# Kernel optimization log

Measured on AMD Instinct MI355X. Metric: run time of the kernel, lower is better.

## Reference

```python
import jax, jax.numpy as jnp
import numpy as np
from jax import lax

B, S, MEL, DM, DI, N, K, R, H, V = 2, 2048, 80, 512, 1024, 16, 4, 32, 8, 10000


def setup_inputs() -> dict:
    ks = iter(jax.random.split(jax.random.key(0), 48))
    r = lambda sh, s=0.02: jax.random.normal(next(ks), sh, jnp.float32) * s
    inp = {"mel": jax.random.normal(next(ks), (B, S, MEL), jnp.float32)}
    inp["mel_w"] = r((DM, MEL)); inp["mel_b"] = r((DM,))
    inp["attn_in_w"] = r((3 * DM, DM)); inp["attn_in_b"] = r((3 * DM,))
    inp["attn_out_w"] = r((DM, DM)); inp["attn_out_b"] = r((DM,))
    inp["ln1_g"] = jnp.ones((DM,)); inp["ln1_b"] = jnp.zeros((DM,))
    inp["ln2_g"] = jnp.ones((DM,)); inp["ln2_b"] = jnp.zeros((DM,))
    for p in ("fm", "bm"):
        inp[p + "_in_w"] = r((2 * DI, DM))
        inp[p + "_conv_w"] = r((DI, K), 0.2)
        inp[p + "_conv_b"] = r((DI,), 0.1)
        inp[p + "_x_w"] = r((R + 2 * N, DI))
        inp[p + "_dt_w"] = r((DI, R), 0.1)
        inp[p + "_dt_b"] = r((DI,), 0.1)
        inp[p + "_A_log"] = jnp.log(jnp.tile(jnp.arange(1, N + 1, dtype=jnp.float32), (DI, 1)))
        inp[p + "_D"] = jnp.ones((DI,))
        inp[p + "_out_w"] = r((DM, DI))
    inp["bim_w"] = r((DM, 2 * DM)); inp["bim_b"] = r((DM,))
    inp["out_w"] = r((V, DM)); inp["out_b"] = r((V,))
    return inp


def _ln(x, g, b):
    mu = x.mean(-1, keepdims=True)
    var = ((x - mu) ** 2).mean(-1, keepdims=True)
    return (x - mu) * lax.rsqrt(var + 1e-5) * g + b


def _mha(x, in_w, in_b, out_w, out_b):
    # torch nn.MultiheadAttention default batch_first=False:
    # axis0 = sequence (here the batch dim B), axis1 = batch (here S). Faithful to source.
    L, Nb, E = x.shape
    hd = E // H
    qkv = x @ in_w.T + in_b
    q, k, v = jnp.split(qkv, 3, axis=-1)
    q = q.reshape(L, Nb, H, hd)
    k = k.reshape(L, Nb, H, hd)
    v = v.reshape(L, Nb, H, hd)
    sc = jnp.einsum('lnhd,mnhd->nhlm', q, k) / np.float32(np.sqrt(hd))
    a = jax.nn.softmax(sc, axis=-1)
    o = jnp.einsum('nhlm,mnhd->lnhd', a, v).reshape(L, Nb, E)
    return o @ out_w.T + out_b


def _mamba(x, in_w, conv_w, conv_b, x_w, dt_w, dt_b, A_log, Dp, out_w):
    # mamba_ssm Mamba block: in_proj -> causal depthwise conv + silu -> x_proj ->
    # softplus(dt_proj) -> selective scan -> gate by silu(z) -> out_proj
    Bb, L, _ = x.shape
    xa, z = jnp.split(x @ in_w.T, 2, axis=-1)  # [B,L,DI] each
    xc = lax.conv_general_dilated(xa.transpose(0, 2, 1), conv_w[:, None, :], (1,), [(K - 1, 0)],
                                  dimension_numbers=('NCH', 'OIH', 'NCH'), feature_group_count=DI)
    xc = jax.nn.silu(xc + conv_b[None, :, None]).transpose(0, 2, 1)  # [B,L,DI]
    dbl = xc @ x_w.T  # [B,L,R+2N]
    dt, Bm, Cm = dbl[..., :R], dbl[..., R:R + N], dbl[..., R + N:]
    dt = jax.nn.softplus(dt @ dt_w.T + dt_b)  # [B,L,DI]
    A = -jnp.exp(A_log)  # [DI,N]

    def step(h, ins):
        dt_t, B_t, C_t, x_t = ins  # [B,DI],[B,N],[B,N],[B,DI]
        h = jnp.exp(dt_t[..., None] * A) * h + (dt_t * x_t)[..., None] * B_t[:, None, :]
        return h, jnp.einsum('bdn,bn->bd', h, C_t)

    h0 = jnp.zeros((Bb, DI, N), x.dtype)
    _, ys = lax.scan(step, h0, (dt.transpose(1, 0, 2), Bm.transpose(1, 0, 2),
                                Cm.transpose(1, 0, 2), xc.transpose(1, 0, 2)))
    y = ys.transpose(1, 0, 2) + xc * Dp
    y = y * jax.nn.silu(z)
    return y @ out_w.T


def reference(mel, mel_w, mel_b, attn_in_w, attn_in_b, attn_out_w, attn_out_b,
              ln1_g, ln1_b, ln2_g, ln2_b,
              fm_in_w, fm_conv_w, fm_conv_b, fm_x_w, fm_dt_w, fm_dt_b, fm_A_log, fm_D, fm_out_w,
              bm_in_w, bm_conv_w, bm_conv_b, bm_x_w, bm_dt_w, bm_dt_b, bm_A_log, bm_D, bm_out_w,
              bim_w, bim_b, out_w, out_b):
    x = mel @ mel_w.T + mel_b  # [B,S,DM]
    x = _ln(x + _mha(x, attn_in_w, attn_in_b, attn_out_w, attn_out_b), ln1_g, ln1_b)
    fwd = _mamba(x, fm_in_w, fm_conv_w, fm_conv_b, fm_x_w, fm_dt_w, fm_dt_b, fm_A_log, fm_D, fm_out_w)
    bwd = jnp.flip(_mamba(jnp.flip(x, 1), bm_in_w, bm_conv_w, bm_conv_b, bm_x_w, bm_dt_w, bm_dt_b, bm_A_log, bm_D, bm_out_w), 1)
    m = jnp.concatenate([fwd, bwd], axis=-1) @ bim_w.T + bim_b
    x = _ln(x + m, ln2_g, ln2_b)
    return x @ out_w.T + out_b  # [B,S,V]
```

## Files before the change

### kernel.cpp

```cpp
#include <hip/hip_runtime.h>
#include <hip/hip_bf16.h>
#include <math.h>

#define SEQ 2048

typedef __attribute__((ext_vector_type(4))) float f32x4;
typedef __attribute__((ext_vector_type(8))) short bf16x8s;
typedef __attribute__((ext_vector_type(8))) unsigned short ushort8;
typedef __attribute__((ext_vector_type(2))) unsigned int uint2v;

__device__ __forceinline__ short f2bf(float f) {
  union { float f; unsigned u; } c; c.f = f;
  unsigned u = c.u;
  u += 0x7fffu + ((u >> 16) & 1u);
  return (short)(u >> 16);
}
__device__ __forceinline__ float bf2f(unsigned short u) {
  union { unsigned u; float f; } c; c.u = ((unsigned)u) << 16; return c.f;
}

__device__ __forceinline__ void lds_load16(const void* g, void* s) {
  __builtin_amdgcn_global_load_lds(
      (const __attribute__((address_space(1))) void*)g,
      (__attribute__((address_space(3))) void*)s, 16, 0, 0);
}

template<int EPI, int OUTBF, int AFLIP1 = 0>
__launch_bounds__(256)
__global__ void gemm_bf16(const unsigned short* A, const unsigned short* B,
                          void* Cv, const float* __restrict__ bias,
                          int M, int N, int K, int lda, int ldb, int ldc, int nbn,
                          const unsigned short* A1, const unsigned short* B1, void* C1) {
  __shared__ char smem[67584];

  if (blockIdx.y) { A = A1; B = B1; Cv = C1; }
  const bool aflip = AFLIP1 && blockIdx.y;

  const int nwg = gridDim.x;
  const int g = blockIdx.x;
  const int q = nwg >> 3, r = nwg & 7;
  const int xcd = g & 7, cidx = g >> 3;
  const int wg = (xcd < r ? xcd * (q + 1) : r * (q + 1) + (xcd - r) * q) + cidx;
  const int sup = nbn << 2;
  const int bmg = wg / sup, rem = wg % sup;
  const int bn = rem >> 2;
  const int bm = (bmg << 2) + (rem & 3);
  const int m0 = bm * 128, n0 = bn * 128;

  const int tid = threadIdx.x, lane = tid & 63, wave = tid >> 6;
  const int wr = (wave >> 1) * 64, wc = (wave & 1) * 64;
  const int fr = lane & 15, fq = lane >> 4;
  const int srow = tid >> 3;
  const int scc  = tid & 7;

  f32x4 acc[4][4] = {};
  const int nkt = K >> 6;

  auto STAGE = [&](int buf, int kt) {
    const int k0 = kt << 6;
    unsigned short* sAb = (unsigned short*)(smem + buf * 32768);
    unsigned short* sBb = (unsigned short*)(smem + buf * 32768 + 16384);
    #pragma unroll
    for (int j = 0; j < 4; j++) {
      int lrow = j * 32 + srow;
      int gcol = (scc ^ (lrow & 7)) * 8;
      int arow = m0 + lrow;
      if (AFLIP1) {
        if (aflip) arow = (arow & ~(SEQ - 1)) | ((SEQ - 1) - (arow & (SEQ - 1)));
      }
      lds_load16(A + (size_t)arow * lda + k0 + gcol, &sAb[(j * 256 + wave * 64) * 8]);
    }
    #pragma unroll
    for (int j = 0; j < 4; j++) {
      int lrow = j * 32 + srow;
      int gcol = (scc ^ (lrow & 7)) * 8;
      int grow = n0 + lrow; if (grow >= N) grow = N - 1;
      lds_load16(B + (size_t)grow * ldb + k0 + gcol, &sBb[(j * 256 + wave * 64) * 8]);
    }
  };

  STAGE(0, 0);

  int cur = 0;
  for (int kt = 0; kt < nkt; kt++) {
    if (kt + 1 < nkt) {
      STAGE(cur ^ 1, kt + 1);
      asm volatile("s_waitcnt vmcnt(8)" ::: "memory");
    } else {
      asm volatile("s_waitcnt vmcnt(0)" ::: "memory");
    }
    __builtin_amdgcn_s_barrier();
    __builtin_amdgcn_sched_barrier(0);
    const unsigned short* As = (const unsigned short*)(smem + cur * 32768);
    const unsigned short* Bs = (const unsigned short*)(smem + cur * 32768 + 16384);
    #pragma unroll
    for (int ks = 0; ks < 2; ks++) {
      bf16x8s af[4], bfv[4];
      #pragma unroll
      for (int i = 0; i < 4; i++) {
        int ra = wr + i * 16 + fr;
        af[i] = *(const bf16x8s*)&As[ra * 64 + (((ks << 2) + fq) ^ (ra & 7)) * 8];
      }
      #pragma unroll
      for (int i = 0; i < 4; i++) {
        int rb = wc + i * 16 + fr;
        bfv[i] = *(const bf16x8s*)&Bs[rb * 64 + (((ks << 2) + fq) ^ (rb & 7)) * 8];
      }
      #pragma unroll
      for (int i = 0; i < 4; i++)
        #pragma unroll
        for (int j = 0; j < 4; j++)
          acc[i][j] = __builtin_amdgcn_mfma_f32_16x16x32_bf16(af[i], bfv[j], acc[i][j], 0, 0, 0);
    }
    __builtin_amdgcn_s_barrier();
    cur ^= 1;
  }

  float* ct = (float*)smem;
  #pragma unroll
  for (int i = 0; i < 4; i++)
    #pragma unroll
    for (int j = 0; j < 4; j++)
      #pragma unroll
      for (int r4 = 0; r4 < 4; r4++)
        ct[(wr + i * 16 + fq * 4 + r4) * 132 + wc + j * 16 + fr] = acc[i][j][r4];
  __syncthreads();
  const int half = lane >> 5;
  const int col4 = (lane & 31) * 4;
  const int cn = n0 + col4;
  #pragma unroll
  for (int it = 0; it < 16; it++) {
    int row = wave * 32 + it * 2 + half;
    f32x4 v = *(const f32x4*)&ct[row * 132 + col4];
    if (cn < N) {
      if (EPI >= 1) {
        f32x4 b4 = *(const f32x4*)&bias[cn];
        #pragma unroll
        for (int j = 0; j < 4; j++) v[j] += b4[j];
      }
      if (OUTBF) {
        unsigned short h0 = (unsigned short)f2bf(v[0]), h1 = (unsigned short)f2bf(v[1]);
        unsigned short h2 = (unsigned short)f2bf(v[2]), h3 = (unsigned short)f2bf(v[3]);
        uint2v o = { (unsigned)h0 | ((unsigned)h1 << 16), (unsigned)h2 | ((unsigned)h3 << 16) };
        *(uint2v*)((unsigned short*)Cv + (size_t)(m0 + row) * ldc + cn) = o;
      } else {
        float* dst = (float*)Cv + (size_t)(m0 + row) * ldc + cn;
        if (EPI == 1) __builtin_nontemporal_store(v, (f32x4*)dst);
        else          *(f32x4*)dst = v;
      }
    }
  }
}

__launch_bounds__(512)
__global__ void dt_kernel(const float* __restrict__ dbl0, const float* __restrict__ dtw0,
                          const float* __restrict__ dtb0, unsigned short* __restrict__ out0,
                          const float* __restrict__ dbl1, const float* __restrict__ dtw1,
                          const float* __restrict__ dtb1, unsigned short* __restrict__ out1) {
  const int dir = blockIdx.y;
  const float* dbl = dir ? dbl1 : dbl0;
  const float* dtw = dir ? dtw1 : dtw0;
  const float* dtb = dir ? dtb1 : dtb0;
  unsigned short* out = dir ? out1 : out0;
  const int t = threadIdx.x;
  const int d0 = t * 2;
  const int m0 = blockIdx.x * 16;
  float w0[32], w1[32];
  #pragma unroll
  for (int qq = 0; qq < 8; qq++) {
    f32x4 v0 = *(const f32x4*)(dtw + (size_t)d0 * 32 + qq * 4);
    f32x4 v1 = *(const f32x4*)(dtw + (size_t)(d0 + 1) * 32 + qq * 4);
    #pragma unroll
    for (int j = 0; j < 4; j++) { w0[qq * 4 + j] = v0[j]; w1[qq * 4 + j] = v1[j]; }
  }
  const float b0 = dtb[d0], b1 = dtb[d0 + 1];
  for (int mi = 0; mi < 16; mi++) {
    const float* dr = dbl + (size_t)(m0 + mi) * 64;
    float a0 = b0, a1 = b1;
    #pragma unroll
    for (int qq = 0; qq < 8; qq++) {
      f32x4 v = *(const f32x4*)(dr + qq * 4);
      #pragma unroll
      for (int j = 0; j < 4; j++) { a0 += v[j] * w0[qq * 4 + j]; a1 += v[j] * w1[qq * 4 + j]; }
    }
    a0 = fmaxf(a0, 0.f) + log1pf(__expf(-fabsf(a0)));
    a1 = fmaxf(a1, 0.f) + log1pf(__expf(-fabsf(a1)));
    unsigned pk = (unsigned)(unsigned short)f2bf(a0) | ((unsigned)(unsigned short)f2bf(a1) << 16);
    *(unsigned*)(out + (size_t)(m0 + mi) * 1024 + d0) = pk;
  }
}

struct CvtArgs { const float* s[14]; unsigned short* d[14]; int n[14]; int pad[14]; };
__global__ void cvt_many(CvtArgs a) {
  int y = blockIdx.y;
  if (a.pad[y]) {
    int idx = blockIdx.x * 256 + threadIdx.x;
    int c = idx & 15, row = idx >> 4;
    if (row >= a.n[y]) return;
    const float* s = a.s[y];
    ushort8 o = { 0, 0, 0, 0, 0, 0, 0, 0 };
    if (c < 10) {
      f32x4 v0 = *(const f32x4*)(s + (size_t)row * 80 + c * 8);
      f32x4 v1 = *(const f32x4*)(s + (size_t)row * 80 + c * 8 + 4);
      o[0] = (unsigned short)f2bf(v0[0]); o[1] = (unsigned short)f2bf(v0[1]);
      o[2] = (unsigned short)f2bf(v0[2]); o[3] = (unsigned short)f2bf(v0[3]);
      o[4] = (unsigned short)f2bf(v1[0]); o[5] = (unsigned short)f2bf(v1[1]);
      o[6] = (unsigned short)f2bf(v1[2]); o[7] = (unsigned short)f2bf(v1[3]);
    }
    *(ushort8*)(a.d[y] + (size_t)row * 128 + c * 8) = o;
    return;
  }
  int i = (blockIdx.x * 256 + threadIdx.x) * 8;
  if (i >= a.n[y]) return;
  const float* s = a.s[y];
  f32x4 v0 = *(const f32x4*)(s + i);
  f32x4 v1 = *(const f32x4*)(s + i + 4);
  ushort8 o = { (unsigned short)f2bf(v0[0]), (unsigned short)f2bf(v0[1]),
                (unsigned short)f2bf(v0[2]), (unsigned short)f2bf(v0[3]),
                (unsigned short)f2bf(v1[0]), (unsigned short)f2bf(v1[1]),
                (unsigned short)f2bf(v1[2]), (unsigned short)f2bf(v1[3]) };
  *(ushort8*)(a.d[y] + i) = o;
}

__global__ void attn_kernel(const unsigned short* __restrict__ qkv, unsigned short* __restrict__ o) {
  int gw = blockIdx.x * 4 + (threadIdx.x >> 6);
  int lane = threadIdx.x & 63;
  int n = gw >> 3, h = gw & 7;
  size_t r0 = (size_t)n * 1536 + h * 64 + lane;
  size_t r1 = (size_t)(SEQ + n) * 1536 + h * 64 + lane;
  float q0 = bf2f(qkv[r0]), k0 = bf2f(qkv[r0 + 512]), v0 = bf2f(qkv[r0 + 1024]);
  float q1 = bf2f(qkv[r1]), k1 = bf2f(qkv[r1 + 512]), v1 = bf2f(qkv[r1 + 1024]);
  float s00 = q0 * k0, s01 = q0 * k1, s10 = q1 * k0, s11 = q1 * k1;
  #pragma unroll
  for (int off = 32; off > 0; off >>= 1) {
    s00 += __shfl_xor(s00, off);
    s01 += __shfl_xor(s01, off);
    s10 += __shfl_xor(s10, off);
    s11 += __shfl_xor(s11, off);
  }
  const float sc = 0.125f;
  s00 *= sc; s01 *= sc; s10 *= sc; s11 *= sc;
  float mx0 = fmaxf(s00, s01), mx1 = fmaxf(s10, s11);
  float e00 = __expf(s00 - mx0), e01 = __expf(s01 - mx0);
  float e10 = __expf(s10 - mx1), e11 = __expf(s11 - mx1);
  float i0 = 1.f / (e00 + e01), i1 = 1.f / (e10 + e11);
  size_t w0 = (size_t)n * 512 + h * 64 + lane;
  size_t w1 = (size_t)(SEQ + n) * 512 + h * 64 + lane;
  o[w0] = (unsigned short)f2bf((e00 * v0 + e01 * v1) * i0);
  o[w1] = (unsigned short)f2bf((e10 * v0 + e11 * v1) * i1);
}

__global__ void ln_res_kernel(const unsigned short* __restrict__ a, const unsigned short* __restrict__ b,
                              const float* __restrict__ g, const float* __restrict__ be,
                              unsigned short* __restrict__ out) {
  int row = blockIdx.x * 4 + (threadIdx.x >> 6);
  int lane = threadIdx.x & 63;
  ushort8 va = *(const ushort8*)(a + (size_t)row * 512 + lane * 8);
  ushort8 vb = *(const ushort8*)(b + (size_t)row * 512 + lane * 8);
  float v[8];
  #pragma unroll
  for (int j = 0; j < 8; j++) v[j] = bf2f(va[j]) + bf2f(vb[j]);
  float s = 0.f, s2 = 0.f;
  #pragma unroll
  for (int j = 0; j < 8; j++) { s += v[j]; s2 += v[j] * v[j]; }
  #pragma unroll
  for (int off = 32; off > 0; off >>= 1) { s += __shfl_xor(s, off); s2 += __shfl_xor(s2, off); }
  float mu = s * (1.f / 512.f);
  float var = s2 * (1.f / 512.f) - mu * mu;
  float rs = rsqrtf(var + 1e-5f);
  const float* pg = g + lane * 8;
  const float* pe = be + lane * 8;
  ushort8 o;
  #pragma unroll
  for (int j = 0; j < 8; j++) o[j] = (unsigned short)f2bf((v[j] - mu) * rs * pg[j] + pe[j]);
  *(ushort8*)(out + (size_t)row * 512 + lane * 8) = o;
}

struct ConvArgs {
  const unsigned short* xz[2];
  const float* w[2];
  const float* cb[2];
  unsigned short* xc[2];
};
__global__ void conv_silu_kernel(ConvArgs a) {
  int dir = blockIdx.y;
  int idx = blockIdx.x * 256 + threadIdx.x;
  int dc = (idx & 127) * 8;
  int t  = (idx >> 7) & (SEQ - 1);
  int b  = idx >> 18;
  const float* w = a.w[dir];
  f32x4 wv[8];
  #pragma unroll
  for (int j = 0; j < 8; j++) wv[j] = *(const f32x4*)(w + (dc + j) * 4);
  float acc[8];
  f32x4 cb0 = *(const f32x4*)(a.cb[dir] + dc), cb1 = *(const f32x4*)(a.cb[dir] + dc + 4);
  #pragma unroll
  for (int j = 0; j < 4; j++) { acc[j] = cb0[j]; acc[4 + j] = cb1[j]; }
  const unsigned short* base = a.xz[dir] + ((size_t)b * SEQ) * 2048 + dc;
  #pragma unroll
  for (int k = 0; k < 4; k++) {
    int tt = t - 3 + k;
    if (tt >= 0) {
      ushort8 xv = *(const ushort8*)(base + (size_t)tt * 2048);
      #pragma unroll
      for (int j = 0; j < 8; j++) acc[j] += wv[j][k] * bf2f(xv[j]);
    }
  }
  ushort8 o;
  #pragma unroll
  for (int j = 0; j < 8; j++) {
    float v = acc[j];
    o[j] = (unsigned short)f2bf(v / (1.f + __expf(-v)));
  }
  *(ushort8*)(a.xc[dir] + (size_t)idx * 8) = o;
}

#define CL 32
#define NC 64

struct ScanArgs {
  const unsigned short* xc[2];
  const float* dbl[2];
  const float* A_log[2];
  const unsigned short* dt[2];
  const float* Dp[2];
  const unsigned short* xz[2];
  float* hend[2];
  float* apr[2];
  float* h0[2];
  unsigned short* ys[2];
};

__global__ void scan_p1(ScanArgs s) {
  int dir = blockIdx.y;
  int tid = blockIdx.x * 256 + threadIdx.x;
  int nq = tid & 3;
  int d = (tid >> 2) & 1023;
  int c = (tid >> 12) & (NC - 1);
  int b = tid >> 18;
  f32x4 va = *(const f32x4*)(s.A_log[dir] + d * 16 + nq * 4);
  float A[4];
  #pragma unroll
  for (int j = 0; j < 4; j++) A[j] = -__expf(va[j]);
  float h[4] = {};
  float ap[4] = { 1.f, 1.f, 1.f, 1.f };
  const unsigned short* xcp = s.xc[dir] + ((size_t)b * SEQ) * 1024 + d;
  const unsigned short* dtp = s.dt[dir] + ((size_t)b * SEQ) * 1024 + d;
  const float* dbp = s.dbl[dir] + ((size_t)b * SEQ) * 64;
  const int t0 = c * CL;
  for (int t = t0; t < t0 + CL; t++) {
    float dtv = bf2f(dtp[(size_t)t * 1024]);
    float dx = dtv * bf2f(xcp[(size_t)t * 1024]);
    f32x4 Bv = *(const f32x4*)(dbp + (size_t)t * 64 + 32 + nq * 4);
    #pragma unroll
    for (int j = 0; j < 4; j++) {
      float e = __expf(dtv * A[j]);
      h[j] = e * h[j] + dx * Bv[j];
      ap[j] *= e;
    }
  }
  size_t o = ((size_t)((b * NC + c) * 1024 + d)) * 16 + nq * 4;
  f32x4 vh = { h[0], h[1], h[2], h[3] };
  f32x4 vap = { ap[0], ap[1], ap[2], ap[3] };
  *(f32x4*)(s.hend[dir] + o) = vh;
  *(f32x4*)(s.apr[dir] + o) = vap;
}

__global__ void scan_p2(ScanArgs s) {
  int dir = blockIdx.y;
  int tid = blockIdx.x * 256 + threadIdx.x;
  int n = tid & 15;
  int d = (tid >> 4) & 1023;
  int b = tid >> 14;
  const float* hend = s.hend[dir];
  const float* apr  = s.apr[dir];
  float* h0 = s.h0[dir];
  float h = 0.f;
  #pragma unroll 8
  for (int c = 0; c < NC; c++) {
    size_t idx = ((size_t)((b * NC + c) * 1024 + d)) * 16 + n;
    h0[idx] = h;
    h = apr[idx] * h + hend[idx];
  }
}

__global__ void scan_p3(ScanArgs s) {
  int dir = blockIdx.y;
  int tid = blockIdx.x * 256 + threadIdx.x;
  int nq = tid & 3;
  int d = (tid >> 2) & 1023;
  int c = (tid >> 12) & (NC - 1);
  int b = tid >> 18;
  f32x4 va = *(const f32x4*)(s.A_log[dir] + d * 16 + nq * 4);
  float A[4];
  #pragma unroll
  for (int j = 0; j < 4; j++) A[j] = -__expf(va[j]);
  const float Dv = s.Dp[dir][d];
  size_t o = ((size_t)((b * NC + c) * 1024 + d)) * 16 + nq * 4;
  f32x4 h4 = *(const f32x4*)(s.h0[dir] + o);
  float h[4] = { h4[0], h4[1], h4[2], h4[3] };
  const unsigned short* xcp = s.xc[dir] + ((size_t)b * SEQ) * 1024 + d;
  const unsigned short* dtp = s.dt[dir] + ((size_t)b * SEQ) * 1024 + d;
  const unsigned short* zp  = s.xz[dir] + ((size_t)b * SEQ) * 2048 + 1024 + d;
  const float* dbp = s.dbl[dir] + ((size_t)b * SEQ) * 64;
  unsigned short* ysp = s.ys[dir] + ((size_t)b * SEQ) * 1024 + d;
  const int t0 = c * CL;
  for (int t = t0; t < t0 + CL; t++) {
    float dtv = bf2f(dtp[(size_t)t * 1024]);
    float xcv = bf2f(xcp[(size_t)t * 1024]);
    float dx = dtv * xcv;
    f32x4 Bv = *(const f32x4*)(dbp + (size_t)t * 64 + 32 + nq * 4);
    f32x4 Cv = *(const f32x4*)(dbp + (size_t)t * 64 + 48 + nq * 4);
    float y = 0.f;
    #pragma unroll
    for (int j = 0; j < 4; j++) {
      float e = __expf(dtv * A[j]);
      h[j] = e * h[j] + dx * Bv[j];
      y += h[j] * Cv[j];
    }
    y += __shfl_xor(y, 1);
    y += __shfl_xor(y, 2);
    if (nq == 0) {
      float z = bf2f(zp[(size_t)t * 2048]);
      float out = (y + xcv * Dv) * (z / (1.f + __expf(-z)));
      int tw = dir ? (SEQ - 1 - t) : t;
      ysp[(size_t)tw * 1024] = (unsigned short)f2bf(out);
    }
  }
}

extern "C" void kernel_launch(void* const* d_in, const int* in_sizes, int n_in,
                              void* d_out, int out_size, void* d_ws, size_t ws_size,
                              hipStream_t stream) {
  (void)in_sizes; (void)n_in; (void)out_size; (void)ws_size;
  const float* mel        = (const float*)d_in[0];
  const float* mel_w      = (const float*)d_in[1];
  const float* mel_b      = (const float*)d_in[2];
  const float* attn_in_b  = (const float*)d_in[4];
  const float* attn_out_b = (const float*)d_in[6];
  const float* ln1_g = (const float*)d_in[7];
  const float* ln1_b = (const float*)d_in[8];
  const float* ln2_g = (const float*)d_in[9];
  const float* ln2_b = (const float*)d_in[10];
  const float* bim_b = (const float*)d_in[30];
  const float* out_b = (const float*)d_in[32];

  char* wsb = (char*)d_ws;
  char* obb = (char*)d_out;

  unsigned short* w_attn_in  = (unsigned short*)(wsb + 0);
  unsigned short* w_attn_out = (unsigned short*)(wsb + 1572864);
  unsigned short* w_dir[2][4];
  for (int dir = 0; dir < 2; dir++) {
    size_t base = 2097152 + (size_t)dir * 3342336;
    w_dir[dir][0] = (unsigned short*)(wsb + base);
    w_dir[dir][1] = (unsigned short*)(wsb + base + 2097152);
    w_dir[dir][2] = (unsigned short*)(wsb + base + 2228224);
    w_dir[dir][3] = (unsigned short*)(wsb + base + 2293760);
  }
  unsigned short* w_bim = (unsigned short*)(wsb + 8781824);
  unsigned short* w_out = (unsigned short*)(wsb + 9830400);

  unsigned short* x0     = (unsigned short*)(wsb + 20971520);
  unsigned short* x1     = (unsigned short*)(wsb + 25165824);
  unsigned short* attn_o = (unsigned short*)(wsb + 33554432);
  unsigned short* xc0    = (unsigned short*)(wsb + 37748736);
  unsigned short* ysb0   = (unsigned short*)(wsb + 46137344);
  unsigned short* mout   = (unsigned short*)(wsb + 62914560);
  unsigned short* minter = (unsigned short*)(wsb + 71303168);
  unsigned short* x2     = (unsigned short*)(wsb + 75497472);
  float*          dbl0   = (float*)(wsb + 79691776);
  unsigned short* melp   = (unsigned short*)(wsb + 80740352);
  unsigned short* melwp  = (unsigned short*)(wsb + 81788928);

  unsigned short* qkv  = (unsigned short*)(obb + 0);
  unsigned short* xz0  = (unsigned short*)(obb + 12582912);
  unsigned short* xz1  = (unsigned short*)(obb + 29360128);
  unsigned short* xc1  = (unsigned short*)(obb + 46137344);
  unsigned short* ysb1 = (unsigned short*)(obb + 54525952);
  float* hend0 = (float*)(obb + 62914560);
  float* hend1 = (float*)(obb + 71303168);
  float* apr0  = (float*)(obb + 79691776);
  float* apr1  = (float*)(obb + 88080384);
  float* h0s0  = (float*)(obb + 96468992);
  float* h0s1  = (float*)(obb + 104857600);
  float* dbl1  = (float*)(obb + 113246208);
  unsigned short* dtf0 = (unsigned short*)(obb + 114294784);
  unsigned short* dtf1 = (unsigned short*)(obb + 122683392);
  float* ob    = (float*)d_out;

  dim3 blk(256);

  {
    CvtArgs a;
    const float* srcs[14] = { (const float*)d_in[3], (const float*)d_in[5],
      (const float*)d_in[11], (const float*)d_in[14], (const float*)d_in[15], (const float*)d_in[19],
      (const float*)d_in[20], (const float*)d_in[23], (const float*)d_in[24], (const float*)d_in[28],
      (const float*)d_in[29], (const float*)d_in[31], mel, mel_w };
    unsigned short* dsts[14] = { w_attn_in, w_attn_out,
      w_dir[0][0], w_dir[0][1], w_dir[0][2], w_dir[0][3],
      w_dir[1][0], w_dir[1][1], w_dir[1][2], w_dir[1][3],
      w_bim, w_out, melp, melwp };
    int ns[14] = { 786432, 262144, 1048576, 65536, 32768, 524288,
                   1048576, 65536, 32768, 524288, 524288, 5120000, 4096, 512 };
    int pads[14] = { 0,0,0,0,0,0,0,0,0,0,0,0,1,1 };
    for (int i = 0; i < 14; i++) { a.s[i] = srcs[i]; a.d[i] = dsts[i]; a.n[i] = ns[i]; a.pad[i] = pads[i]; }
    cvt_many<<<dim3(2500, 14), blk, 0, stream>>>(a);
  }

  gemm_bf16<1, 1><<<dim3(4 * 32), blk, 0, stream>>>(melp, melwp, x0, mel_b,
      4096, 512, 128, 128, 128, 512, 4, nullptr, nullptr, nullptr);
  gemm_bf16<1, 1><<<dim3(12 * 32), blk, 0, stream>>>(x0, w_attn_in, qkv, attn_in_b,
      4096, 1536, 512, 512, 512, 1536, 12, nullptr, nullptr, nullptr);
  attn_kernel<<<4096, blk, 0, stream>>>(qkv, attn_o);
  gemm_bf16<1, 1><<<dim3(4 * 32), blk, 0, stream>>>(attn_o, w_attn_out, qkv, attn_out_b,
      4096, 512, 512, 512, 512, 512, 4, nullptr, nullptr, nullptr);
  ln_res_kernel<<<1024, blk, 0, stream>>>(x0, qkv, ln1_g, ln1_b, x1);

  ScanArgs sa;
  ConvArgs ca;
  for (int dir = 0; dir < 2; dir++) {
    int base = 11 + dir * 9;
    ca.xz[dir] = dir ? xz1 : xz0;
    ca.w[dir]  = (const float*)d_in[base + 1];
    ca.cb[dir] = (const float*)d_in[base + 2];
    ca.xc[dir] = dir ? xc1 : xc0;
    sa.xc[dir]    = dir ? xc1 : xc0;
    sa.dbl[dir]   = dir ? dbl1 : dbl0;
    sa.A_log[dir] = (const float*)d_in[base + 6];
    sa.dt[dir]    = dir ? dtf1 : dtf0;
    sa.Dp[dir]    = (const float*)d_in[base + 7];
    sa.xz[dir]    = dir ? xz1 : xz0;
    sa.hend[dir]  = dir ? hend1 : hend0;
    sa.apr[dir]   = dir ? apr1 : apr0;
    sa.h0[dir]    = dir ? h0s1 : h0s0;
    sa.ys[dir]    = dir ? ysb1 : ysb0;
  }
  gemm_bf16<0, 1, 1><<<dim3(16 * 32, 2), blk, 0, stream>>>(x1, w_dir[0][0], xz0, nullptr,
      4096, 2048, 512, 512, 512, 2048, 16, x1, w_dir[1][0], xz1);
  conv_silu_kernel<<<dim3(2048, 2), blk, 0, stream>>>(ca);
  gemm_bf16<0, 0><<<dim3(1 * 32, 2), blk, 0, stream>>>(xc0, w_dir[0][1], dbl0, nullptr,
      4096, 64, 1024, 1024, 1024, 64, 1, xc1, w_dir[1][1], dbl1);
  dt_kernel<<<dim3(256, 2), dim3(512), 0, stream>>>(
      dbl0, (const float*)d_in[15], (const float*)d_in[16], dtf0,
      dbl1, (const float*)d_in[24], (const float*)d_in[25], dtf1);
  scan_p1<<<dim3(2048, 2), blk, 0, stream>>>(sa);
  scan_p2<<<dim3(128, 2), blk, 0, stream>>>(sa);
  scan_p3<<<dim3(2048, 2), blk, 0, stream>>>(sa);
  gemm_bf16<0, 1><<<dim3(4 * 32, 2), blk, 0, stream>>>(ysb0, w_dir[0][3], mout, nullptr,
      4096, 512, 1024, 1024, 1024, 1024, 4, ysb1, w_dir[1][3], mout + 512);

  gemm_bf16<1, 1><<<dim3(4 * 32), blk, 0, stream>>>(mout, w_bim, minter, bim_b,
      4096, 512, 1024, 1024, 1024, 512, 4, nullptr, nullptr, nullptr);
  ln_res_kernel<<<1024, blk, 0, stream>>>(x1, minter, ln2_g, ln2_b, x2);
  gemm_bf16<1, 0><<<dim3(79 * 32), blk, 0, stream>>>(x2, w_out, ob, out_b,
      4096, 10000, 512, 512, 512, 10000, 79, nullptr, nullptr, nullptr);
}
```

Before: 359.3 us.

## Halve GEMM LDS footprint with 32-wide K tiles and two-pass epilogue

Result: slower. 375.8 us (+4.6%).

```diff
diff --git a/kernel.cpp b/kernel.cpp
--- a/kernel.cpp
+++ b/kernel.cpp
@@ -31,7 +31,7 @@
                           void* Cv, const float* __restrict__ bias,
                           int M, int N, int K, int lda, int ldb, int ldc, int nbn,
                           const unsigned short* A1, const unsigned short* B1, void* C1) {
-  __shared__ char smem[67584];
+  __shared__ char smem[33792];
 
   if (blockIdx.y) { A = A1; B = B1; Cv = C1; }
   const bool aflip = AFLIP1 && blockIdx.y;
@@ -50,32 +50,28 @@
   const int tid = threadIdx.x, lane = tid & 63, wave = tid >> 6;
   const int wr = (wave >> 1) * 64, wc = (wave & 1) * 64;
   const int fr = lane & 15, fq = lane >> 4;
-  const int srow = tid >> 3;
-  const int scc  = tid & 7;
 
   f32x4 acc[4][4] = {};
-  const int nkt = K >> 6;
+  const int nkt = K >> 5;
 
   auto STAGE = [&](int buf, int kt) {
-    const int k0 = kt << 6;
-    unsigned short* sAb = (unsigned short*)(smem + buf * 32768);
-    unsigned short* sBb = (unsigned short*)(smem + buf * 32768 + 16384);
-    #pragma unroll
-    for (int j = 0; j < 4; j++) {
-      int lrow = j * 32 + srow;
-      int gcol = (scc ^ (lrow & 7)) * 8;
+    const int k0 = kt << 5;
+    char* base = smem + buf * 16384;
+    const int gcol = (lane & 3) * 8;
+    #pragma unroll
+    for (int j = 0; j < 2; j++) {
+      int lrow = j * 64 + wave * 16 + (lane >> 2);
       int arow = m0 + lrow;
       if (AFLIP1) {
         if (aflip) arow = (arow & ~(SEQ - 1)) | ((SEQ - 1) - (arow & (SEQ - 1)));
       }
-      lds_load16(A + (size_t)arow * lda + k0 + gcol, &sAb[(j * 256 + wave * 64) * 8]);
-    }
-    #pragma unroll
-    for (int j = 0; j < 4; j++) {
-      int lrow = j * 32 + srow;
-      int gcol = (scc ^ (lrow & 7)) * 8;
+      lds_load16(A + (size_t)arow * lda + k0 + gcol, base + j * 4096 + wave * 1024);
+    }
+    #pragma unroll
+    for (int j = 0; j < 2; j++) {
+      int lrow = j * 64 + wave * 16 + (lane >> 2);
       int grow = n0 + lrow; if (grow >= N) grow = N - 1;
-      lds_load16(B + (size_t)grow * ldb + k0 + gcol, &sBb[(j * 256 + wave * 64) * 8]);
+      lds_load16(B + (size_t)grow * ldb + k0 + gcol, base + 8192 + j * 4096 + wave * 1024);
     }
   };
 
@@ -85,70 +81,70 @@
   for (int kt = 0; kt < nkt; kt++) {
     if (kt + 1 < nkt) {
       STAGE(cur ^ 1, kt + 1);
-      asm volatile("s_waitcnt vmcnt(8)" ::: "memory");
+      asm volatile("s_waitcnt vmcnt(4)" ::: "memory");
     } else {
       asm volatile("s_waitcnt vmcnt(0)" ::: "memory");
     }
     __builtin_amdgcn_s_barrier();
     __builtin_amdgcn_sched_barrier(0);
-    const unsigned short* As = (const unsigned short*)(smem + cur * 32768);
-    const unsigned short* Bs = (const unsigned short*)(smem + cur * 32768 + 16384);
-    #pragma unroll
-    for (int ks = 0; ks < 2; ks++) {
-      bf16x8s af[4], bfv[4];
+    const unsigned short* As = (const unsigned short*)(smem + cur * 16384);
+    const unsigned short* Bs = (const unsigned short*)(smem + cur * 16384 + 8192);
+    bf16x8s af[4], bfv[4];
+    #pragma unroll
+    for (int i = 0; i < 4; i++)
+      af[i] = *(const bf16x8s*)&As[(wr + i * 16 + fr) * 32 + fq * 8];
+    #pragma unroll
+    for (int i = 0; i < 4; i++)
+      bfv[i] = *(const bf16x8s*)&Bs[(wc + i * 16 + fr) * 32 + fq * 8];
+    #pragma unroll
+    for (int i = 0; i < 4; i++)
       #pragma unroll
-      for (int i = 0; i < 4; i++) {
-        int ra = wr + i * 16 + fr;
-        af[i] = *(const bf16x8s*)&As[ra * 64 + (((ks << 2) + fq) ^ (ra & 7)) * 8];
-      }
-      #pragma unroll
-      for (int i = 0; i < 4; i++) {
-        int rb = wc + i * 16 + fr;
-        bfv[i] = *(const bf16x8s*)&Bs[rb * 64 + (((ks << 2) + fq) ^ (rb & 7)) * 8];
-      }
+      for (int j = 0; j < 4; j++)
+        acc[i][j] = __builtin_amdgcn_mfma_f32_16x16x32_bf16(af[i], bfv[j], acc[i][j], 0, 0, 0);
+    __builtin_amdgcn_s_barrier();
+    cur ^= 1;
+  }
+
+  float* ct = (float*)smem;
+  const int half = lane >> 5;
+  const int col4 = (lane & 31) * 4;
+  const int cn = n0 + col4;
+  #pragma unroll
+  for (int h = 0; h < 2; h++) {
+    if ((wave >> 1) == h) {
       #pragma unroll
       for (int i = 0; i < 4; i++)
         #pragma unroll
         for (int j = 0; j < 4; j++)
-          acc[i][j] = __builtin_amdgcn_mfma_f32_16x16x32_bf16(af[i], bfv[j], acc[i][j], 0, 0, 0);
-    }
-    __builtin_amdgcn_s_barrier();
-    cur ^= 1;
-  }
-
-  float* ct = (float*)smem;
-  #pragma unroll
-  for (int i = 0; i < 4; i++)
-    #pragma unroll
-    for (int j = 0; j < 4; j++)
-      #pragma unroll
-      for (int r4 = 0; r4 < 4; r4++)
-        ct[(wr + i * 16 + fq * 4 + r4) * 132 + wc + j * 16 + fr] = acc[i][j][r4];
-  __syncthreads();
-  const int half = lane >> 5;
-  const int col4 = (lane & 31) * 4;
-  const int cn = n0 + col4;
-  #pragma unroll
-  for (int it = 0; it < 16; it++) {
-    int row = wave * 32 + it * 2 + half;
-    f32x4 v = *(const f32x4*)&ct[row * 132 + col4];
-    if (cn < N) {
-      if (EPI >= 1) {
-        f32x4 b4 = *(const f32x4*)&bias[cn];
-        #pragma unroll
-        for (int j = 0; j < 4; j++) v[j] += b4[j];
+          #pragma unroll
+          for (int r4 = 0; r4 < 4; r4++)
+            ct[(i * 16 + fq * 4 + r4) * 132 + wc + j * 16 + fr] = acc[i][j][r4];
+    }
+    __syncthreads();
+    #pragma unroll
+    for (int it = 0; it < 8; it++) {
+      int row2 = wave * 16 + it * 2 + half;
+      f32x4 v = *(const f32x4*)&ct[row2 * 132 + col4];
+      if (cn < N) {
+        if (EPI >= 1) {
+          f32x4 b4 = *(const f32x4*)&bias[cn];
+          #pragma unroll
+          for (int j = 0; j < 4; j++) v[j] += b4[j];
+        }
+        int grow = m0 + h * 64 + row2;
+        if (OUTBF) {
+          unsigned short h0 = (unsigned short)f2bf(v[0]), h1 = (unsigned short)f2bf(v[1]);
+          unsigned short h2 = (unsigned short)f2bf(v[2]), h3 = (unsigned short)f2bf(v[3]);
+          uint2v o = { (unsigned)h0 | ((unsigned)h1 << 16), (unsigned)h2 | ((unsigned)h3 << 16) };
+          *(uint2v*)((unsigned short*)Cv + (size_t)grow * ldc + cn) = o;
+        } else {
+          float* dst = (float*)Cv + (size_t)grow * ldc + cn;
+          if (EPI == 1) __builtin_nontemporal_store(v, (f32x4*)dst);
+          else          *(f32x4*)dst = v;
+        }
       }
-      if (OUTBF) {
-        unsigned short h0 = (unsigned short)f2bf(v[0]), h1 = (unsigned short)f2bf(v[1]);
-        unsigned short h2 = (unsigned short)f2bf(v[2]), h3 = (unsigned short)f2bf(v[3]);
-        uint2v o = { (unsigned)h0 | ((unsigned)h1 << 16), (unsigned)h2 | ((unsigned)h3 << 16) };
-        *(uint2v*)((unsigned short*)Cv + (size_t)(m0 + row) * ldc + cn) = o;
-      } else {
-        float* dst = (float*)Cv + (size_t)(m0 + row) * ldc + cn;
-        if (EPI == 1) __builtin_nontemporal_store(v, (f32x4*)dst);
-        else          *(f32x4*)dst = v;
-      }
-    }
+    }
+    __syncthreads();
   }
 }
 
```

## Single-buffer GEMM LDS and split epilogue to halve shared memory

Applied to the files above, without the earlier changes.

New measurement: 413.5 us. 15.1% more time.

```diff
diff --git a/kernel.cpp b/kernel.cpp
--- a/kernel.cpp
+++ b/kernel.cpp
@@ -31,7 +31,7 @@
                           void* Cv, const float* __restrict__ bias,
                           int M, int N, int K, int lda, int ldb, int ldc, int nbn,
                           const unsigned short* A1, const unsigned short* B1, void* C1) {
-  __shared__ char smem[67584];
+  __shared__ char smem[33792];
 
   if (blockIdx.y) { A = A1; B = B1; Cv = C1; }
   const bool aflip = AFLIP1 && blockIdx.y;
@@ -55,11 +55,11 @@
 
   f32x4 acc[4][4] = {};
   const int nkt = K >> 6;
-
-  auto STAGE = [&](int buf, int kt) {
+  unsigned short* sA = (unsigned short*)smem;
+  unsigned short* sB = (unsigned short*)(smem + 16384);
+
+  for (int kt = 0; kt < nkt; kt++) {
     const int k0 = kt << 6;
-    unsigned short* sAb = (unsigned short*)(smem + buf * 32768);
-    unsigned short* sBb = (unsigned short*)(smem + buf * 32768 + 16384);
     #pragma unroll
     for (int j = 0; j < 4; j++) {
       int lrow = j * 32 + srow;
@@ -68,43 +68,28 @@
       if (AFLIP1) {
         if (aflip) arow = (arow & ~(SEQ - 1)) | ((SEQ - 1) - (arow & (SEQ - 1)));
       }
-      lds_load16(A + (size_t)arow * lda + k0 + gcol, &sAb[(j * 256 + wave * 64) * 8]);
+      lds_load16(A + (size_t)arow * lda + k0 + gcol, &sA[(j * 256 + wave * 64) * 8]);
     }
     #pragma unroll
     for (int j = 0; j < 4; j++) {
       int lrow = j * 32 + srow;
       int gcol = (scc ^ (lrow & 7)) * 8;
       int grow = n0 + lrow; if (grow >= N) grow = N - 1;
-      lds_load16(B + (size_t)grow * ldb + k0 + gcol, &sBb[(j * 256 + wave * 64) * 8]);
-    }
-  };
-
-  STAGE(0, 0);
-
-  int cur = 0;
-  for (int kt = 0; kt < nkt; kt++) {
-    if (kt + 1 < nkt) {
-      STAGE(cur ^ 1, kt + 1);
-      asm volatile("s_waitcnt vmcnt(8)" ::: "memory");
-    } else {
-      asm volatile("s_waitcnt vmcnt(0)" ::: "memory");
-    }
-    __builtin_amdgcn_s_barrier();
-    __builtin_amdgcn_sched_barrier(0);
-    const unsigned short* As = (const unsigned short*)(smem + cur * 32768);
-    const unsigned short* Bs = (const unsigned short*)(smem + cur * 32768 + 16384);
+      lds_load16(B + (size_t)grow * ldb + k0 + gcol, &sB[(j * 256 + wave * 64) * 8]);
+    }
+    __syncthreads();
     #pragma unroll
     for (int ks = 0; ks < 2; ks++) {
       bf16x8s af[4], bfv[4];
       #pragma unroll
       for (int i = 0; i < 4; i++) {
         int ra = wr + i * 16 + fr;
-        af[i] = *(const bf16x8s*)&As[ra * 64 + (((ks << 2) + fq) ^ (ra & 7)) * 8];
+        af[i] = *(const bf16x8s*)&sA[ra * 64 + (((ks << 2) + fq) ^ (ra & 7)) * 8];
       }
       #pragma unroll
       for (int i = 0; i < 4; i++) {
         int rb = wc + i * 16 + fr;
-        bfv[i] = *(const bf16x8s*)&Bs[rb * 64 + (((ks << 2) + fq) ^ (rb & 7)) * 8];
+        bfv[i] = *(const bf16x8s*)&sB[rb * 64 + (((ks << 2) + fq) ^ (rb & 7)) * 8];
       }
       #pragma unroll
       for (int i = 0; i < 4; i++)
@@ -112,43 +97,49 @@
         for (int j = 0; j < 4; j++)
           acc[i][j] = __builtin_amdgcn_mfma_f32_16x16x32_bf16(af[i], bfv[j], acc[i][j], 0, 0, 0);
     }
-    __builtin_amdgcn_s_barrier();
-    cur ^= 1;
+    __syncthreads();
   }
 
   float* ct = (float*)smem;
-  #pragma unroll
-  for (int i = 0; i < 4; i++)
-    #pragma unroll
-    for (int j = 0; j < 4; j++)
-      #pragma unroll
-      for (int r4 = 0; r4 < 4; r4++)
-        ct[(wr + i * 16 + fq * 4 + r4) * 132 + wc + j * 16 + fr] = acc[i][j][r4];
-  __syncthreads();
   const int half = lane >> 5;
   const int col4 = (lane & 31) * 4;
   const int cn = n0 + col4;
   #pragma unroll
-  for (int it = 0; it < 16; it++) {
-    int row = wave * 32 + it * 2 + half;
-    f32x4 v = *(const f32x4*)&ct[row * 132 + col4];
-    if (cn < N) {
-      if (EPI >= 1) {
-        f32x4 b4 = *(const f32x4*)&bias[cn];
+  for (int h = 0; h < 2; h++) {
+    if ((wave >> 1) == h) {
+      #pragma unroll
+      for (int i = 0; i < 4; i++)
         #pragma unroll
-        for (int j = 0; j < 4; j++) v[j] += b4[j];
+        for (int j = 0; j < 4; j++)
+          #pragma unroll
+          for (int r4 = 0; r4 < 4; r4++)
+            ct[(i * 16 + fq * 4 + r4) * 132 + wc + j * 16 + fr] = acc[i][j][r4];
+    }
+    __syncthreads();
+    #pragma unroll
+    for (int it = 0; it < 8; it++) {
+      int row2 = wave * 16 + it * 2 + half;
+      f32x4 v = *(const f32x4*)&ct[row2 * 132 + col4];
+      if (cn < N) {
+        if (EPI >= 1) {
+          f32x4 b4 = *(const f32x4*)&bias[cn];
+          #pragma unroll
+          for (int j = 0; j < 4; j++) v[j] += b4[j];
+        }
+        int grow = m0 + h * 64 + row2;
+        if (OUTBF) {
+          unsigned short h0 = (unsigned short)f2bf(v[0]), h1 = (unsigned short)f2bf(v[1]);
+          unsigned short h2 = (unsigned short)f2bf(v[2]), h3 = (unsigned short)f2bf(v[3]);
+          uint2v o = { (unsigned)h0 | ((unsigned)h1 << 16), (unsigned)h2 | ((unsigned)h3 << 16) };
+          *(uint2v*)((unsigned short*)Cv + (size_t)grow * ldc + cn) = o;
+        } else {
+          float* dst = (float*)Cv + (size_t)grow * ldc + cn;
+          if (EPI == 1) __builtin_nontemporal_store(v, (f32x4*)dst);
+          else          *(f32x4*)dst = v;
+        }
       }
-      if (OUTBF) {
-        unsigned short h0 = (unsigned short)f2bf(v[0]), h1 = (unsigned short)f2bf(v[1]);
-        unsigned short h2 = (unsigned short)f2bf(v[2]), h3 = (unsigned short)f2bf(v[3]);
-        uint2v o = { (unsigned)h0 | ((unsigned)h1 << 16), (unsigned)h2 | ((unsigned)h3 << 16) };
-        *(uint2v*)((unsigned short*)Cv + (size_t)(m0 + row) * ldc + cn) = o;
-      } else {
-        float* dst = (float*)Cv + (size_t)(m0 + row) * ldc + cn;
-        if (EPI == 1) __builtin_nontemporal_store(v, (f32x4*)dst);
-        else          *(f32x4*)dst = v;
-      }
-    }
+    }
+    __syncthreads();
   }
 }
 
```
